# Kernel optimization log

Hardware: AMD Instinct MI355X
Metric: run time of the kernel (lower is better)

The kernel has to match this reference:

```python
import jax, jax.numpy as jnp
import numpy as np
from jax.scipy.special import logsumexp

B, S, L = 1024, 8192, 3


def setup_inputs() -> dict:
    key = jax.random.key(0)
    k1, k2, k3, k4, k5 = jax.random.split(key, 5)
    emissions = jax.random.normal(k1, (B, S, L), dtype=jnp.float32)
    labels = jax.random.randint(k2, (B, S), 0, L, dtype=jnp.int64)
    start_transitions = 0.1 * jax.random.normal(k3, (L,), dtype=jnp.float32)
    transitions = 0.1 * jax.random.normal(k4, (L, L), dtype=jnp.float32)
    end_transitions = 0.1 * jax.random.normal(k5, (L,), dtype=jnp.float32)
    return {
        "emissions": emissions,
        "labels": labels,
        "start_transitions": start_transitions,
        "transitions": transitions,
        "end_transitions": end_transitions,
    }


def reference(emissions, labels, start_transitions, transitions, end_transitions):
    # mask is all-ones in the original module, so every timestep is valid.
    # --- log partition via forward algorithm (sequential DP over time) ---
    alpha0 = start_transitions[None, :] + emissions[:, 0]  # [B, L]

    def step(alpha, e_t):
        # alpha: [B, L] (prev label), e_t: [B, L] (next label)
        nxt = logsumexp(alpha[:, :, None] + transitions[None, :, :] + e_t[:, None, :], axis=1)
        return nxt, None

    e_rest = jnp.swapaxes(emissions[:, 1:], 0, 1)  # [S-1, B, L]
    alphaT, _ = jax.lax.scan(step, alpha0, e_rest)
    log_z = logsumexp(alphaT + end_transitions[None, :], axis=-1)  # [B]

    # --- gold path score ---
    em_score = jnp.take_along_axis(emissions, labels[:, :, None], axis=2)[..., 0].sum(axis=1)  # [B]
    trans_score = transitions[labels[:, :-1], labels[:, 1:]].sum(axis=1)  # [B]
    score = start_transitions[labels[:, 0]] + em_score + trans_score + end_transitions[labels[:, -1]]

    log_likelihood = jnp.sum(score - log_z)  # torchcrf default reduction='sum'
    return -log_likelihood
```

## Files before the change

kernel.cpp:

```cpp
#include <hip/hip_runtime.h>

#define LOG2E 1.44269504088896340736f
#define LN2   0.69314718055994530942f
#define S_    8192
#define CHUNK 2048
#define NCH   4
#define TPB   256
#define KPT   8
#define NWAVE 4

#if __has_builtin(__builtin_amdgcn_exp2f)
__device__ __forceinline__ float exp2f_(float x){ return __builtin_amdgcn_exp2f(x); }
#else
__device__ __forceinline__ float exp2f_(float x){ return __expf(x * LN2); }
#endif
#if __has_builtin(__builtin_amdgcn_logf)
__device__ __forceinline__ float log2f_(float x){ return __builtin_amdgcn_logf(x); }
#else
__device__ __forceinline__ float log2f_(float x){ return __logf(x) * LOG2E; }
#endif

__device__ __forceinline__ void gload16(const void* g, void* l, int ln){
#if __has_builtin(__builtin_amdgcn_global_load_lds)
    __builtin_amdgcn_global_load_lds((const __attribute__((address_space(1))) void*)g,
                                     (__attribute__((address_space(3))) void*)l, 16, 0, 0);
#else
    *(float4*)((char*)l + ln*16) = *(const float4*)g;
#endif
}

__device__ __forceinline__ void renorm9(float* V, float& s){
    float m = fmaxf(fmaxf(fmaxf(V[0],V[1]),fmaxf(V[2],V[3])),
                    fmaxf(fmaxf(V[4],V[5]),fmaxf(V[6],V[7])));
    m = fmaxf(m, V[8]);
    int e = (__float_as_int(m) >> 23) & 0xff;
    float rs = __int_as_float((254 - e) << 23);
#pragma unroll
    for (int k=0;k<9;++k) V[k] *= rs;
    s += (float)(e - 127);
}

__device__ __forceinline__ void mul33(float* C, const float* A, const float* B){
#pragma unroll
    for (int i=0;i<3;i++){
        float a0=A[i*3], a1=A[i*3+1], a2=A[i*3+2];
#pragma unroll
        for (int j=0;j<3;j++)
            C[i*3+j] = a0*B[j] + a1*B[3+j] + a2*B[6+j];
    }
}

extern "C" __global__ __launch_bounds__(TPB)
void crf_fwd(const float* __restrict__ em, const int* __restrict__ lab,
             const float* __restrict__ stt, const float* __restrict__ trt,
             const float* __restrict__ ent, float* __restrict__ ws)
{
    const int bid = blockIdx.x;
    const int b = bid >> 2, h = bid & 3;
    const int tid = threadIdx.x, ln = tid & 63, wv = tid >> 6;

    __shared__ float4 emS[CHUNK*3/4];
    __shared__ float  tT[9];
    __shared__ float  wM[NWAVE][10];
    __shared__ float  wSc[NWAVE];

    const float* emB = em + ((size_t)b*S_ + (size_t)h*CHUNK)*3;
    const int*   lbB = lab + (size_t)b*S_ + h*CHUNK;

    {
        const char* gb = (const char*)emB;
        char* lb = (char*)&emS[0];
#pragma unroll
        for (int k=0;k<6;++k){
            int c = k*NWAVE + wv;
            gload16(gb + c*1024 + ln*16, lb + c*1024, ln);
        }
    }
    if (tid < 9) tT[tid] = trt[tid];

    const int4* lb4 = (const int4*)lbB;
    int4 lv0 = lb4[2*tid], lv1 = lb4[2*tid+1];

    float W00=__expf(trt[0]), W01=__expf(trt[1]), W02=__expf(trt[2]);
    float W10=__expf(trt[3]), W11=__expf(trt[4]), W12=__expf(trt[5]);
    float W20=__expf(trt[6]), W21=__expf(trt[7]), W22=__expf(trt[8]);

    const bool head = (h==0 && tid==0);
    int prev_sh = __shfl_up(lv1.w, 1, 64);
    int prev;
    if (ln == 0) prev = head ? 0 : lbB[tid*KPT - 1];
    else         prev = prev_sh;

    __syncthreads();

    float ew[24];
    {
        const float4* p = &emS[tid*6];
        *(float4*)&ew[0]  = p[0]; *(float4*)&ew[4]  = p[1]; *(float4*)&ew[8]  = p[2];
        *(float4*)&ew[12] = p[3]; *(float4*)&ew[16] = p[4]; *(float4*)&ew[20] = p[5];
    }
    int lw[8] = {lv0.x,lv0.y,lv0.z,lv0.w, lv1.x,lv1.y,lv1.z,lv1.w};

    float V[9] = {1,0,0, 0,1,0, 0,0,1};
    float S2 = 0.f, sc = 0.f;
#pragma unroll
    for (int s=0; s<KPT; ++s){
        float ea=ew[3*s], eb=ew[3*s+1], ec=ew[3*s+2];
        int l = lw[s];
        float ee = (l==1) ? eb : ((l==2) ? ec : ea);
        if (head && s==0) sc += stt[l] + ee;
        else              sc += tT[prev*3+l] + ee;
        prev = l;
        if (!(head && s==0)) {
            float E0=__expf(ea), E1=__expf(eb), E2=__expf(ec);
#pragma unroll
            for (int i=0;i<3;i++){
                float a0=V[i*3], a1=V[i*3+1], a2=V[i*3+2];
                V[i*3]  =(a0*W00+a1*W10+a2*W20)*E0;
                V[i*3+1]=(a0*W01+a1*W11+a2*W21)*E1;
                V[i*3+2]=(a0*W02+a1*W12+a2*W22)*E2;
            }
        }
        if (s==3 || s==7) renorm9(V, S2);
    }

#pragma unroll
    for (int off=1; off<64; off<<=1){
        float bv[9];
#pragma unroll
        for (int k=0;k<9;++k) bv[k] = __shfl_down(V[k], (unsigned)off, 64);
        float bs2 = __shfl_down(S2, (unsigned)off, 64);
        float C[9]; mul33(C, V, bv);
        S2 += bs2;
        renorm9(C, S2);
#pragma unroll
        for (int k=0;k<9;++k) V[k]=C[k];
    }
#pragma unroll
    for (int off=32; off; off>>=1) sc += __shfl_down(sc, (unsigned)off, 64);

    if (ln==0){
#pragma unroll
        for (int k=0;k<9;++k) wM[wv][k]=V[k];
        wM[wv][9]=S2; wSc[wv]=sc;
    }
    __syncthreads();

    if (tid==0){
        float A[9], As = wM[0][9], scT = wSc[0];
#pragma unroll
        for (int k=0;k<9;++k) A[k]=wM[0][k];
#pragma unroll
        for (int w=1; w<NWAVE; ++w){
            float C[9]; mul33(C, A, wM[w]);
            As += wM[w][9];
            renorm9(C, As);
#pragma unroll
            for (int k=0;k<9;++k) A[k]=C[k];
            scT += wSc[w];
        }
        float* r = ws + (size_t)bid*16;
#pragma unroll
        for (int k=0;k<9;++k) r[k]=A[k];
        r[9]=As; r[10]=scT;
        r[11]=ew[0]; r[12]=ew[1]; r[13]=ew[2];
    }
}

extern "C" __global__ __launch_bounds__(1024)
void crf_fin(const float* __restrict__ ws, const float* __restrict__ stt,
             const float* __restrict__ ent, float* __restrict__ out, int B)
{
    const int b = threadIdx.x;
    float nll = 0.f;
    if (b < B){
        const float* rr = ws + (size_t)b*NCH*16;
        float C[9], S = rr[9], sc = rr[10];
#pragma unroll
        for (int k=0;k<9;++k) C[k]=rr[k];
#pragma unroll
        for (int q=1;q<NCH;++q){
            const float* r = rr + q*16;
            float T[9]; mul33(T, C, r);
#pragma unroll
            for (int k=0;k<9;++k) C[k]=T[k];
            S += r[9]; sc += r[10];
        }
        float a0=(stt[0]+rr[11])*LOG2E, a1=(stt[1]+rr[12])*LOG2E, a2=(stt[2]+rr[13])*LOG2E;
        float am = fmaxf(fmaxf(a0,a1),a2);
        float w0=exp2f_(a0-am), w1=exp2f_(a1-am), w2=exp2f_(a2-am);
        float q0=w0*C[0]+w1*C[3]+w2*C[6];
        float q1=w0*C[1]+w1*C[4]+w2*C[7];
        float q2=w0*C[2]+w1*C[5]+w2*C[8];
        float z = q0*exp2f_(ent[0]*LOG2E) + q1*exp2f_(ent[1]*LOG2E) + q2*exp2f_(ent[2]*LOG2E);
        float logz = (am + S + log2f_(z)) * LN2;
        nll = logz - sc;
    }
#pragma unroll
    for (int off=32; off; off>>=1) nll += __shfl_down(nll, (unsigned)off, 64);
    __shared__ float acc[16];
    if ((threadIdx.x & 63)==0) acc[threadIdx.x>>6] = nll;
    __syncthreads();
    if (threadIdx.x==0){
        float s=0.f;
#pragma unroll
        for (int k=0;k<16;++k) s += acc[k];
        out[0] = s;
    }
}

extern "C" void kernel_launch(void* const* d_in, const int* in_sizes, int n_in,
                              void* d_out, int out_size, void* d_ws, size_t ws_size,
                              hipStream_t stream) {
    const float* em  = (const float*)d_in[0];
    const int*   lab = (const int*)d_in[1];
    const float* stt = (const float*)d_in[2];
    const float* trt = (const float*)d_in[3];
    const float* ent = (const float*)d_in[4];
    float* out = (float*)d_out;
    float* ws  = (float*)d_ws;

    const int B = in_sizes[1] / S_;
    crf_fwd<<<NCH*B, TPB, 0, stream>>>(em, lab, stt, trt, ent, ws);
    crf_fin<<<1, 1024, 0, stream>>>(ws, stt, ent, out, B);
}
```

Baseline: 191.4 us.

## Use single-wave blocks per 512-step chunk and split final reduction

Each forward block is now a single 64-lane wave that handles a 512-step chunk, so there are 16 chunks per sequence instead of 4. Emissions load directly from global memory into registers instead of being staged through LDS with global_load_lds, and the cross-wave LDS combine step is gone. The finalize stage becomes a 16-block kernel that combines 16 chunk matrices per batch, renormalising after each product, followed by a tiny second reduction kernel. This trades an extra kernel launch and more workspace traffic for more independent blocks, no block-level syncs, and a finalize stage spread over more than one CU.

Result: faster. 184.8 us (-3.5%).

```diff
diff --git a/kernel.cpp b/kernel.cpp
--- a/kernel.cpp
+++ b/kernel.cpp
@@ -3,11 +3,9 @@
 #define LOG2E 1.44269504088896340736f
 #define LN2   0.69314718055994530942f
 #define S_    8192
-#define CHUNK 2048
-#define NCH   4
-#define TPB   256
+#define WCH   512
+#define NCH   16
 #define KPT   8
-#define NWAVE 4
 
 #if __has_builtin(__builtin_amdgcn_exp2f)
 __device__ __forceinline__ float exp2f_(float x){ return __builtin_amdgcn_exp2f(x); }
@@ -19,15 +17,6 @@
 #else
 __device__ __forceinline__ float log2f_(float x){ return __logf(x) * LOG2E; }
 #endif
-
-__device__ __forceinline__ void gload16(const void* g, void* l, int ln){
-#if __has_builtin(__builtin_amdgcn_global_load_lds)
-    __builtin_amdgcn_global_load_lds((const __attribute__((address_space(1))) void*)g,
-                                     (__attribute__((address_space(3))) void*)l, 16, 0, 0);
-#else
-    *(float4*)((char*)l + ln*16) = *(const float4*)g;
-#endif
-}
 
 __device__ __forceinline__ void renorm9(float* V, float& s){
     float m = fmaxf(fmaxf(fmaxf(V[0],V[1]),fmaxf(V[2],V[3])),
@@ -50,55 +39,43 @@
     }
 }
 
-extern "C" __global__ __launch_bounds__(TPB)
+extern "C" __global__ __launch_bounds__(64)
 void crf_fwd(const float* __restrict__ em, const int* __restrict__ lab,
              const float* __restrict__ stt, const float* __restrict__ trt,
              const float* __restrict__ ent, float* __restrict__ ws)
 {
     const int bid = blockIdx.x;
-    const int b = bid >> 2, h = bid & 3;
-    const int tid = threadIdx.x, ln = tid & 63, wv = tid >> 6;
+    const int b = bid >> 4, h = bid & 15;
+    const int ln = threadIdx.x;
 
-    __shared__ float4 emS[CHUNK*3/4];
-    __shared__ float  tT[9];
-    __shared__ float  wM[NWAVE][10];
-    __shared__ float  wSc[NWAVE];
+    __shared__ float tT[9];
 
-    const float* emB = em + ((size_t)b*S_ + (size_t)h*CHUNK)*3;
-    const int*   lbB = lab + (size_t)b*S_ + h*CHUNK;
+    const float* emB = em + ((size_t)b*S_ + (size_t)h*WCH)*3;
+    const int*   lbB = lab + (size_t)b*S_ + h*WCH;
 
-    {
-        const char* gb = (const char*)emB;
-        char* lb = (char*)&emS[0];
-#pragma unroll
-        for (int k=0;k<6;++k){
-            int c = k*NWAVE + wv;
-            gload16(gb + c*1024 + ln*16, lb + c*1024, ln);
-        }
-    }
-    if (tid < 9) tT[tid] = trt[tid];
+    const float4* ep = (const float4*)emB + ln*6;
+    float4 r0=ep[0], r1=ep[1], r2=ep[2], r3=ep[3], r4=ep[4], r5=ep[5];
 
     const int4* lb4 = (const int4*)lbB;
-    int4 lv0 = lb4[2*tid], lv1 = lb4[2*tid+1];
+    int4 lv0 = lb4[2*ln], lv1 = lb4[2*ln+1];
+
+    if (ln < 9) tT[ln] = trt[ln];
 
     float W00=__expf(trt[0]), W01=__expf(trt[1]), W02=__expf(trt[2]);
     float W10=__expf(trt[3]), W11=__expf(trt[4]), W12=__expf(trt[5]);
     float W20=__expf(trt[6]), W21=__expf(trt[7]), W22=__expf(trt[8]);
 
-    const bool head = (h==0 && tid==0);
+    const bool head = (h==0 && ln==0);
     int prev_sh = __shfl_up(lv1.w, 1, 64);
     int prev;
-    if (ln == 0) prev = head ? 0 : lbB[tid*KPT - 1];
+    if (ln == 0) prev = head ? 0 : lbB[-1];
     else         prev = prev_sh;
 
     __syncthreads();
 
     float ew[24];
-    {
-        const float4* p = &emS[tid*6];
-        *(float4*)&ew[0]  = p[0]; *(float4*)&ew[4]  = p[1]; *(float4*)&ew[8]  = p[2];
-        *(float4*)&ew[12] = p[3]; *(float4*)&ew[16] = p[4]; *(float4*)&ew[20] = p[5];
-    }
+    *(float4*)&ew[0]=r0;  *(float4*)&ew[4]=r1;  *(float4*)&ew[8]=r2;
+    *(float4*)&ew[12]=r3; *(float4*)&ew[16]=r4; *(float4*)&ew[20]=r5;
     int lw[8] = {lv0.x,lv0.y,lv0.z,lv0.w, lv1.x,lv1.y,lv1.z,lv1.w};
 
     float V[9] = {1,0,0, 0,1,0, 0,0,1};
@@ -139,74 +116,54 @@
 #pragma unroll
     for (int off=32; off; off>>=1) sc += __shfl_down(sc, (unsigned)off, 64);
 
-    if (ln==0){
-#pragma unroll
-        for (int k=0;k<9;++k) wM[wv][k]=V[k];
-        wM[wv][9]=S2; wSc[wv]=sc;
-    }
-    __syncthreads();
-
-    if (tid==0){
-        float A[9], As = wM[0][9], scT = wSc[0];
-#pragma unroll
-        for (int k=0;k<9;++k) A[k]=wM[0][k];
-#pragma unroll
-        for (int w=1; w<NWAVE; ++w){
-            float C[9]; mul33(C, A, wM[w]);
-            As += wM[w][9];
-            renorm9(C, As);
-#pragma unroll
-            for (int k=0;k<9;++k) A[k]=C[k];
-            scT += wSc[w];
-        }
+    if (ln == 0){
         float* r = ws + (size_t)bid*16;
 #pragma unroll
-        for (int k=0;k<9;++k) r[k]=A[k];
-        r[9]=As; r[10]=scT;
+        for (int k=0;k<9;++k) r[k]=V[k];
+        r[9]=S2; r[10]=sc;
         r[11]=ew[0]; r[12]=ew[1]; r[13]=ew[2];
     }
 }
 
-extern "C" __global__ __launch_bounds__(1024)
-void crf_fin(const float* __restrict__ ws, const float* __restrict__ stt,
-             const float* __restrict__ ent, float* __restrict__ out, int B)
+extern "C" __global__ __launch_bounds__(64)
+void crf_fin1(const float* __restrict__ ws, const float* __restrict__ stt,
+              const float* __restrict__ ent, float* __restrict__ partial)
 {
-    const int b = threadIdx.x;
-    float nll = 0.f;
-    if (b < B){
-        const float* rr = ws + (size_t)b*NCH*16;
-        float C[9], S = rr[9], sc = rr[10];
+    const int q = blockIdx.x*64 + threadIdx.x;
+    const float* rr = ws + (size_t)q*NCH*16;
+    float C[9], S = rr[9], sc = rr[10];
 #pragma unroll
-        for (int k=0;k<9;++k) C[k]=rr[k];
+    for (int k=0;k<9;++k) C[k]=rr[k];
 #pragma unroll
-        for (int q=1;q<NCH;++q){
-            const float* r = rr + q*16;
-            float T[9]; mul33(T, C, r);
+    for (int p=1;p<NCH;++p){
+        const float* r = rr + p*16;
+        float T[9]; mul33(T, C, r);
+        S += r[9]; sc += r[10];
+        renorm9(T, S);
 #pragma unroll
-            for (int k=0;k<9;++k) C[k]=T[k];
-            S += r[9]; sc += r[10];
-        }
-        float a0=(stt[0]+rr[11])*LOG2E, a1=(stt[1]+rr[12])*LOG2E, a2=(stt[2]+rr[13])*LOG2E;
-        float am = fmaxf(fmaxf(a0,a1),a2);
-        float w0=exp2f_(a0-am), w1=exp2f_(a1-am), w2=exp2f_(a2-am);
-        float q0=w0*C[0]+w1*C[3]+w2*C[6];
-        float q1=w0*C[1]+w1*C[4]+w2*C[7];
-        float q2=w0*C[2]+w1*C[5]+w2*C[8];
-        float z = q0*exp2f_(ent[0]*LOG2E) + q1*exp2f_(ent[1]*LOG2E) + q2*exp2f_(ent[2]*LOG2E);
-        float logz = (am + S + log2f_(z)) * LN2;
-        nll = logz - sc;
+        for (int k=0;k<9;++k) C[k]=T[k];
     }
+    float a0=(stt[0]+rr[11])*LOG2E, a1=(stt[1]+rr[12])*LOG2E, a2=(stt[2]+rr[13])*LOG2E;
+    float am = fmaxf(fmaxf(a0,a1),a2);
+    float w0=exp2f_(a0-am), w1=exp2f_(a1-am), w2=exp2f_(a2-am);
+    float q0=w0*C[0]+w1*C[3]+w2*C[6];
+    float q1=w0*C[1]+w1*C[4]+w2*C[7];
+    float q2=w0*C[2]+w1*C[5]+w2*C[8];
+    float z = q0*exp2f_(ent[0]*LOG2E) + q1*exp2f_(ent[1]*LOG2E) + q2*exp2f_(ent[2]*LOG2E);
+    float logz = (am + S + log2f_(z)) * LN2;
+    float nll = logz - sc;
 #pragma unroll
     for (int off=32; off; off>>=1) nll += __shfl_down(nll, (unsigned)off, 64);
-    __shared__ float acc[16];
-    if ((threadIdx.x & 63)==0) acc[threadIdx.x>>6] = nll;
-    __syncthreads();
-    if (threadIdx.x==0){
-        float s=0.f;
+    if (threadIdx.x==0) partial[blockIdx.x] = nll;
+}
+
+extern "C" __global__ __launch_bounds__(64)
+void crf_fin2(const float* __restrict__ partial, float* __restrict__ out)
+{
+    float v = (threadIdx.x < 16) ? partial[threadIdx.x] : 0.f;
 #pragma unroll
-        for (int k=0;k<16;++k) s += acc[k];
-        out[0] = s;
-    }
+    for (int off=32; off; off>>=1) v += __shfl_down(v, (unsigned)off, 64);
+    if (threadIdx.x==0) out[0] = v;
 }
 
 extern "C" void kernel_launch(void* const* d_in, const int* in_sizes, int n_in,
@@ -219,8 +176,10 @@
     const float* ent = (const float*)d_in[4];
     float* out = (float*)d_out;
     float* ws  = (float*)d_ws;
+    const int B = in_sizes[1] / S_;
+    float* partial = ws + (size_t)NCH*B*16;
 
-    const int B = in_sizes[1] / S_;
-    crf_fwd<<<NCH*B, TPB, 0, stream>>>(em, lab, stt, trt, ent, ws);
-    crf_fin<<<1, 1024, 0, stream>>>(ws, stt, ent, out, B);
+    crf_fwd<<<NCH*B, 64, 0, stream>>>(em, lab, stt, trt, ent, ws);
+    crf_fin1<<<B/64, 64, 0, stream>>>(ws, stt, ent, partial);
+    crf_fin2<<<1, 64, 0, stream>>>(partial, out);
 }
```
